# Performance work log

Hardware: AMD Instinct MI355X
Metric: run time of the kernel (lower is better)

## Reference

```python
import jax, jax.numpy as jnp
import numpy as np

B, F, D, H = 16384, 39, 16, 2   # batch, fields, embed_dim, heads
VOCAB = 10000                    # per-field vocab
DH = D * H                       # attention output dim per layer (no head split)


def setup_inputs() -> dict:
    key = jax.random.key(0)
    ks = jax.random.split(key, 32)
    def n(k, shape, s=0.05):
        return jax.random.normal(k, shape, jnp.float32) * s
    inp = {"x": jax.random.randint(ks[0], (B, F), 0, VOCAB, dtype=jnp.int32)}
    inp["emb"] = n(ks[1], (F * VOCAB, D))
    idx = 2
    for i, din in enumerate([D, DH, DH]):  # layer0: 16->32, layers 1-2: 32->32
        for nm in ["wq", "wk", "wv", "wr"]:
            inp[f"{nm}{i}"] = n(ks[idx], (din, DH)); idx += 1
    prev = F * DH  # 1248 after flatten
    for i, u in enumerate([128, 64, 32, 1], 1):
        inp[f"w{i}"] = n(ks[idx], (prev, u)); idx += 1
        inp[f"b{i}"] = jnp.zeros((u,), jnp.float32)
        prev = u
    return inp


def reference(x, emb,
              wq0, wk0, wv0, wr0,
              wq1, wk1, wv1, wr1,
              wq2, wk2, wv2, wr2,
              w1, b1, w2, b2, w3, b3, w4, b4):
    offsets = jnp.arange(F, dtype=jnp.int32) * VOCAB
    e = emb[x + offsets]                                   # [B, F, D]
    for wq, wk, wv, wr in [(wq0, wk0, wv0, wr0),
                           (wq1, wk1, wv1, wr1),
                           (wq2, wk2, wv2, wr2)]:
        q = jnp.einsum('bfd,de->bfe', e, wq)               # [B, F, DH]
        k = jnp.einsum('bfd,de->bfe', e, wk)
        v = jnp.einsum('bfd,de->bfe', e, wv)
        att = jax.nn.softmax(jnp.einsum('bfe,bge->bfg', q, k), axis=-1)  # [B,F,F], no scaling
        out = jnp.einsum('bfg,bge->bfe', att, v) + jnp.einsum('bfd,de->bfe', e, wr)
        e = jax.nn.relu(out)
    h = e.reshape(B, F * DH)
    for w, b in [(w1, b1), (w2, b2), (w3, b3)]:
        h = jax.nn.relu(h @ w + b)
    return jax.nn.sigmoid(h @ w4 + b4)                     # [B, 1]
```

## Files before the change

### kernel.cpp

```cpp
#include <hip/hip_runtime.h>
#include <math.h>

#define NF   39
#define NB   16384
#define NVOC 10000

typedef unsigned short u16;
typedef unsigned int   u32;
typedef float f32x4 __attribute__((ext_vector_type(4)));
typedef short s16x8 __attribute__((ext_vector_type(8)));

#define E3_U16   20447232u
#define NSWZ     182272

__device__ __forceinline__ u32 bfadj(float x){
    u32 u = __float_as_uint(x);
    return u + 0x7fffu + ((u >> 16) & 1u);
}
__device__ __forceinline__ u32 pk2(float a, float b){
#if __has_builtin(__builtin_amdgcn_cvt_pk_bf16_f32)
    auto t = __builtin_amdgcn_cvt_pk_bf16_f32(a, b);
    u32 r; __builtin_memcpy(&r, &t, 4); return r;
#else
    return __builtin_amdgcn_perm(bfadj(a), bfadj(b), 0x03020706u);
#endif
}
__device__ __forceinline__ u16 f2bf(float f){ return (u16)(bfadj(f) >> 16); }

__device__ __forceinline__ void wave_sync(){
    asm volatile("s_waitcnt lgkmcnt(0)" ::: "memory");
}
__device__ __forceinline__ f32x4 mfma16(s16x8 a, s16x8 b, f32x4 c){
    return __builtin_amdgcn_mfma_f32_16x16x32_bf16(a, b, c, 0, 0, 0);
}
__device__ __forceinline__ void store4(u16* p, f32x4 v){
    *(uint2*)p = make_uint2(pk2(v[0], v[1]), pk2(v[2], v[3]));
}

__global__ void __launch_bounds__(256) swz_kernel(
    const float* __restrict__ wq0, const float* __restrict__ wk0,
    const float* __restrict__ wv0, const float* __restrict__ wr0,
    const float* __restrict__ wq1, const float* __restrict__ wk1,
    const float* __restrict__ wv1, const float* __restrict__ wr1,
    const float* __restrict__ wq2, const float* __restrict__ wk2,
    const float* __restrict__ wv2, const float* __restrict__ wr2,
    const float* __restrict__ w1, const float* __restrict__ w2,
    const float* __restrict__ w3, u16* __restrict__ ws)
{
    int gid = (int)blockIdx.x*256 + (int)threadIdx.x;
    if (gid >= NSWZ) return;
    int w    = gid & 511;
    int lane = w >> 3, j = w & 7;
    int n    = lane & 15, quad = lane >> 4;
    int kin  = quad*8 + j;
    float val;
    if (gid < 12288){
        int mat = gid >> 10;
        int nt  = (gid >> 9) & 1;
        const float* W;
        switch (mat){
            case 0: W = wq0; break; case 1: W = wk0; break;
            case 2: W = wv0; break; case 3: W = wr0; break;
            case 4: W = wq1; break; case 5: W = wk1; break;
            case 6: W = wv1; break; case 7: W = wr1; break;
            case 8: W = wq2; break; case 9: W = wk2; break;
            case 10: W = wv2; break; default: W = wr2; break;
        }
        int din = (mat < 4) ? 16 : 32;
        val = (kin < din) ? W[kin*32 + nt*16 + n] : 0.f;
    } else if (gid < 12288 + 159744){
        int tt = (gid - 12288) >> 9;
        int ks = tt >> 3, nt = tt & 7;
        val = w1[(ks*32 + kin)*128 + nt*16 + n];
    } else if (gid < 12288 + 159744 + 8192){
        int tt = (gid - (12288+159744)) >> 9;
        int ks = tt >> 2, nt = tt & 3;
        val = w2[(ks*32 + kin)*64 + nt*16 + n];
    } else {
        int tt = (gid - (12288+159744+8192)) >> 9;
        int ks = tt >> 1, nt = tt & 1;
        val = w3[(ks*32 + kin)*32 + nt*16 + n];
    }
    ws[E3_U16 + gid] = f2bf(val);
}

__global__ void __launch_bounds__(256, 3) attn_kernel(
    const int* __restrict__ x, const float* __restrict__ emb,
    u16* __restrict__ ws)
{
    __shared__ __align__(16) u16 lds[4*6656];
    const int tid  = (int)threadIdx.x;
    const int wid  = tid >> 6, lane = tid & 63;
    const int h    = lane >> 4, nl = lane & 15;
    const int r    = (int)blockIdx.x*4 + wid;

    u16* eBuf = lds + wid*6656;
    u16* kBuf = eBuf + 1536;
    u16* qBuf = kBuf + 1536;
    u16* vBuf = qBuf + 1536;
    u16* pBuf = kBuf;
    const u16* wmat = ws + E3_U16;
    const f32x4 z = {0.f, 0.f, 0.f, 0.f};
    const int A_off = nl*8 + (h>>1)*128 + (h&1)*4;

    f32x4 ci;
#pragma unroll
    for (int reg = 0; reg < 4; ++reg)
        ci[reg] = (h*4 + reg >= 7) ? -1e30f : 0.f;

    if (lane < 48){
        int f = lane, mt = f >> 4, fl = f & 15;
        u16* row = eBuf + mt*512 + fl*8;
        if (f < NF){
            const float4* ep = (const float4*)(emb + ((size_t)(x[r*NF + f] + f*NVOC))*16);
            float4 e0 = ep[0], e1 = ep[1], e2 = ep[2], e3 = ep[3];
            *(uint4*)(row)       = make_uint4(pk2(e0.x,e0.y), pk2(e0.z,e0.w),
                                              pk2(e1.x,e1.y), pk2(e1.z,e1.w));
            *(uint4*)(row + 128) = make_uint4(pk2(e2.x,e2.y), pk2(e2.z,e2.w),
                                              pk2(e3.x,e3.y), pk2(e3.z,e3.w));
        } else {
            *(uint4*)(row)       = make_uint4(0,0,0,0);
            *(uint4*)(row + 128) = make_uint4(0,0,0,0);
        }
        *(uint4*)(row + 256) = make_uint4(0,0,0,0);
        *(uint4*)(row + 384) = make_uint4(0,0,0,0);
    }
    wave_sync();

#pragma unroll 1
    for (int L = 0; L < 3; ++L){
        const u16* wB = wmat + L*4096;
        s16x8 bE[3];
#pragma unroll
        for (int nt = 0; nt < 3; ++nt)
            bE[nt] = *(const s16x8*)(eBuf + nt*512 + lane*8);

        {
            s16x8 a0 = *(const s16x8*)(wB + lane*8);
            s16x8 a1 = *(const s16x8*)(wB + 512 + lane*8);
#pragma unroll
            for (int nt = 0; nt < 3; ++nt){
                store4(qBuf + nt*512       + A_off, mfma16(a0, bE[nt], z));
                store4(qBuf + nt*512 + 256 + A_off, mfma16(a1, bE[nt], z));
            }
        }
        {
            s16x8 a0 = *(const s16x8*)(wB + 1024 + lane*8);
            s16x8 a1 = *(const s16x8*)(wB + 1536 + lane*8);
#pragma unroll
            for (int nt = 0; nt < 3; ++nt){
                store4(kBuf + nt*512       + A_off, mfma16(a0, bE[nt], z));
                store4(kBuf + nt*512 + 256 + A_off, mfma16(a1, bE[nt], z));
            }
        }
        {
            s16x8 b0 = *(const s16x8*)(wB + 2048 + lane*8);
            s16x8 b1 = *(const s16x8*)(wB + 2560 + lane*8);
#pragma unroll
            for (int mtg = 0; mtg < 3; ++mtg){
                int toff = (mtg>>1)*1024 + (mtg&1)*256;
                store4(vBuf + toff       + A_off, mfma16(bE[mtg], b0, z));
                store4(vBuf + toff + 512 + A_off, mfma16(bE[mtg], b1, z));
            }
            *(uint2*)(vBuf + 2*512 + 256 + lane*4) = make_uint2(0,0);
            *(uint2*)(vBuf + 3*512 + 256 + lane*4) = make_uint2(0,0);
        }
        f32x4 R[2][3];
        {
            s16x8 a0 = *(const s16x8*)(wB + 3072 + lane*8);
            s16x8 a1 = *(const s16x8*)(wB + 3584 + lane*8);
#pragma unroll
            for (int nt = 0; nt < 3; ++nt){
                R[0][nt] = mfma16(a0, bE[nt], z);
                R[1][nt] = mfma16(a1, bE[nt], z);
            }
        }
        wave_sync();

        f32x4 S[3][3];
        {
            s16x8 aK[3], bQ[3];
#pragma unroll
            for (int i = 0; i < 3; ++i){
                aK[i] = *(const s16x8*)(kBuf + i*512 + lane*8);
                bQ[i] = *(const s16x8*)(qBuf + i*512 + lane*8);
            }
#pragma unroll
            for (int mtg = 0; mtg < 3; ++mtg)
#pragma unroll
            for (int nt = 0; nt < 3; ++nt)
                S[mtg][nt] = mfma16(aK[mtg], bQ[nt], (mtg == 2) ? ci : z);
        }
        float inv[3];
#pragma unroll
        for (int nt = 0; nt < 3; ++nt){
            float t = 0.f;
#pragma unroll
            for (int mtg = 0; mtg < 3; ++mtg)
#pragma unroll
            for (int reg = 0; reg < 4; ++reg){
                S[mtg][nt][reg] = __expf(S[mtg][nt][reg]);
                t += S[mtg][nt][reg];
            }
            t += __shfl_xor(t, 16, 64);
            t += __shfl_xor(t, 32, 64);
            inv[nt] = 1.0f / t;
        }
#pragma unroll
        for (int mtg = 0; mtg < 3; ++mtg)
#pragma unroll
        for (int nt = 0; nt < 3; ++nt)
            store4(pBuf + ((mtg>>1)*3 + nt)*512 + (mtg&1)*256 + A_off, S[mtg][nt]);
        wave_sync();

        s16x8 aV[2][2], bP[2][3];
#pragma unroll
        for (int ks = 0; ks < 2; ++ks){
#pragma unroll
            for (int emt = 0; emt < 2; ++emt)
                aV[ks][emt] = *(const s16x8*)(vBuf + (ks*2+emt)*512 + lane*8);
#pragma unroll
            for (int nt = 0; nt < 3; ++nt)
                bP[ks][nt] = *(const s16x8*)(pBuf + (ks*3+nt)*512 + lane*8);
        }
        if (L < 2){
#pragma unroll
            for (int emt = 0; emt < 2; ++emt)
#pragma unroll
            for (int nt = 0; nt < 3; ++nt){
                f32x4 o = mfma16(aV[1][emt], bP[1][nt],
                         mfma16(aV[0][emt], bP[0][nt], z));
                float m = (nt < 2 || nl < 7) ? 1.f : 0.f;
#pragma unroll
                for (int reg = 0; reg < 4; ++reg)
                    o[reg] = fmaxf(fmaf(o[reg], inv[nt], R[emt][nt][reg]), 0.f) * m;
                store4(eBuf + nt*512 + emt*256 + A_off, o);
            }
        } else {
            int st = r >> 4, sm = r & 15;
            u32 base = (u32)(st*39)*512u + (u32)(sm*8 + (h>>1)*128 + (h&1)*4);
#pragma unroll
            for (int emt = 0; emt < 2; ++emt)
#pragma unroll
            for (int nt = 0; nt < 3; ++nt){
                f32x4 o = mfma16(aV[1][emt], bP[1][nt],
                         mfma16(aV[0][emt], bP[0][nt], z));
#pragma unroll
                for (int reg = 0; reg < 4; ++reg)
                    o[reg] = fmaxf(fmaf(o[reg], inv[nt], R[emt][nt][reg]), 0.f);
                int f = nt*16 + nl;
                if (f < NF)
                    *(uint2*)(ws + base + (u32)f*512u + emt*256) =
                        make_uint2(pk2(o[0], o[1]), pk2(o[2], o[3]));
            }
        }
        wave_sync();
    }
}

__global__ void __launch_bounds__(256, 4) mlp_kernel(
    const float* __restrict__ b1, const float* __restrict__ b2,
    const float* __restrict__ b3, const float* __restrict__ w4,
    const float* __restrict__ b4, const u16* __restrict__ ws,
    float* __restrict__ out)
{
    __shared__ __align__(16) float red[8192];
    __shared__ __align__(16) u16 h1t[2048];
    __shared__ __align__(16) u16 h2t[1024];
    __shared__ float part[32];
    const int tid = (int)threadIdx.x;
    const int w   = tid >> 6, lane = tid & 63;
    const int h   = lane >> 4, nl = lane & 15;
    const int st  = (int)blockIdx.x;
    const int A_off = nl*8 + (h>>1)*128 + (h&1)*4;

    const u16* w1b = ws + E3_U16 + 12288u;
    const u16* w2b = w1b + 159744u;
    const u16* w3b = w2b + 8192u;
    const f32x4 z = {0.f,0.f,0.f,0.f};

    f32x4 acc[8];
#pragma unroll
    for (int nt = 0; nt < 8; ++nt) acc[nt] = z;
#pragma unroll 1
    for (int ks = w; ks < 39; ks += 4){
        s16x8 aE = *(const s16x8*)(ws + (u32)(st*39 + ks)*512u + lane*8);
#pragma unroll
        for (int nt = 0; nt < 8; ++nt){
            s16x8 aW = *(const s16x8*)(w1b + (ks*8 + nt)*512 + lane*8);
            acc[nt] = mfma16(aW, aE, acc[nt]);
        }
    }
#pragma unroll
    for (int nt = 0; nt < 8; ++nt)
        *(f32x4*)(red + (w*8 + nt)*256 + lane*4) = acc[nt];
    __syncthreads();

#pragma unroll
    for (int t = 0; t < 2; ++t){
        int ft = 2*w + t;
        f32x4 s = *(const f32x4*)(red + (0*8 + ft)*256 + lane*4);
#pragma unroll
        for (int p = 1; p < 4; ++p){
            f32x4 q = *(const f32x4*)(red + (p*8 + ft)*256 + lane*4);
#pragma unroll
            for (int reg = 0; reg < 4; ++reg) s[reg] += q[reg];
        }
        float4 bv = *(const float4*)(b1 + ft*16 + h*4);
        f32x4 v;
        v[0] = fmaxf(s[0] + bv.x, 0.f);
        v[1] = fmaxf(s[1] + bv.y, 0.f);
        v[2] = fmaxf(s[2] + bv.z, 0.f);
        v[3] = fmaxf(s[3] + bv.w, 0.f);
        store4(h1t + ft*256 + A_off, v);
    }
    __syncthreads();

    {
        f32x4 a2 = z;
#pragma unroll
        for (int ks = 0; ks < 4; ++ks){
            s16x8 aW = *(const s16x8*)(w2b + (ks*4 + w)*512 + lane*8);
            s16x8 bH = *(const s16x8*)(h1t + ks*512 + lane*8);
            a2 = mfma16(aW, bH, a2);
        }
        float4 bv = *(const float4*)(b2 + w*16 + h*4);
        f32x4 v;
        v[0] = fmaxf(a2[0] + bv.x, 0.f);
        v[1] = fmaxf(a2[1] + bv.y, 0.f);
        v[2] = fmaxf(a2[2] + bv.z, 0.f);
        v[3] = fmaxf(a2[3] + bv.w, 0.f);
        store4(h2t + (w>>1)*512 + (w&1)*256 + A_off, v);
    }
    __syncthreads();

    if (w < 2){
        f32x4 a3 = z;
#pragma unroll
        for (int ks = 0; ks < 2; ++ks){
            s16x8 aW = *(const s16x8*)(w3b + (ks*2 + w)*512 + lane*8);
            s16x8 bH = *(const s16x8*)(h2t + ks*512 + lane*8);
            a3 = mfma16(aW, bH, a3);
        }
        float4 b3v = *(const float4*)(b3 + w*16 + h*4);
        float4 w4v = *(const float4*)(w4 + w*16 + h*4);
        float t = fmaxf(a3[0] + b3v.x, 0.f)*w4v.x
                + fmaxf(a3[1] + b3v.y, 0.f)*w4v.y
                + fmaxf(a3[2] + b3v.z, 0.f)*w4v.z
                + fmaxf(a3[3] + b3v.w, 0.f)*w4v.w;
        t += __shfl_xor(t, 16, 64);
        t += __shfl_xor(t, 32, 64);
        if (h == 0) part[w*16 + nl] = t;
    }
    __syncthreads();
    if (tid < 16){
        float zz = part[tid] + part[16 + tid] + b4[0];
        out[st*16 + tid] = 1.f/(1.f + __expf(-zz));
    }
}

extern "C" void kernel_launch(void* const* d_in, const int* in_sizes, int n_in,
                              void* d_out, int out_size, void* d_ws, size_t ws_size,
                              hipStream_t stream)
{
    (void)in_sizes; (void)n_in; (void)ws_size; (void)out_size;
    const int*   x   = (const int*)d_in[0];
    const float* emb = (const float*)d_in[1];
    u16* ws = (u16*)d_ws;

    swz_kernel<<<(NSWZ+255)/256, 256, 0, stream>>>(
        (const float*)d_in[2],  (const float*)d_in[3],  (const float*)d_in[4],  (const float*)d_in[5],
        (const float*)d_in[6],  (const float*)d_in[7],  (const float*)d_in[8],  (const float*)d_in[9],
        (const float*)d_in[10], (const float*)d_in[11], (const float*)d_in[12], (const float*)d_in[13],
        (const float*)d_in[14], (const float*)d_in[16], (const float*)d_in[18], ws);

    attn_kernel<<<NB/4, 256, 0, stream>>>(x, emb, ws);

    mlp_kernel<<<NB/16, 256, 0, stream>>>(
        (const float*)d_in[15], (const float*)d_in[17], (const float*)d_in[19],
        (const float*)d_in[20], (const float*)d_in[21], ws, (float*)d_out);
}
```

Baseline: 192.1 us.

## Shrink attention LDS footprint, fold log2e into Wq, accumulate residual in MFMA

Overlaps the embedding buffer with the V buffer, cutting per-wave LDS from 6656 to 5120 elements so launch bounds can rise to 4 blocks per CU. Extra waits are added so the aliased buffer is not overwritten before it is read. Log2(e) is folded into the Wq weights during swizzling so softmax can use the hardware exp2, and the reciprocal uses a fast rcp. Probabilities are normalised before the PV MFMA so the residual R can seed the accumulator directly. This costs some bf16 precision on the normalised probabilities and the folded Wq.

```diff
diff --git a/kernel.cpp b/kernel.cpp
--- a/kernel.cpp
+++ b/kernel.cpp
@@ -26,6 +26,21 @@
 #endif
 }
 __device__ __forceinline__ u16 f2bf(float f){ return (u16)(bfadj(f) >> 16); }
+
+__device__ __forceinline__ float fexp2(float x){
+#if __has_builtin(__builtin_amdgcn_exp2f)
+    return __builtin_amdgcn_exp2f(x);
+#else
+    return exp2f(x);
+#endif
+}
+__device__ __forceinline__ float frcp(float x){
+#if __has_builtin(__builtin_amdgcn_rcpf)
+    return __builtin_amdgcn_rcpf(x);
+#else
+    return 1.f / x;
+#endif
+}
 
 __device__ __forceinline__ void wave_sync(){
     asm volatile("s_waitcnt lgkmcnt(0)" ::: "memory");
@@ -68,6 +83,7 @@
         }
         int din = (mat < 4) ? 16 : 32;
         val = (kin < din) ? W[kin*32 + nt*16 + n] : 0.f;
+        if ((mat & 3) == 0) val *= 1.44269504f;
     } else if (gid < 12288 + 159744){
         int tt = (gid - 12288) >> 9;
         int ks = tt >> 3, nt = tt & 7;
@@ -84,20 +100,20 @@
     ws[E3_U16 + gid] = f2bf(val);
 }
 
-__global__ void __launch_bounds__(256, 3) attn_kernel(
+__global__ void __launch_bounds__(256, 4) attn_kernel(
     const int* __restrict__ x, const float* __restrict__ emb,
     u16* __restrict__ ws)
 {
-    __shared__ __align__(16) u16 lds[4*6656];
+    __shared__ __align__(16) u16 lds[4*5120];
     const int tid  = (int)threadIdx.x;
     const int wid  = tid >> 6, lane = tid & 63;
     const int h    = lane >> 4, nl = lane & 15;
     const int r    = (int)blockIdx.x*4 + wid;
 
-    u16* eBuf = lds + wid*6656;
-    u16* kBuf = eBuf + 1536;
+    u16* vBuf = lds + wid*5120;
+    u16* eBuf = vBuf;
+    u16* kBuf = vBuf + 2048;
     u16* qBuf = kBuf + 1536;
-    u16* vBuf = qBuf + 1536;
     u16* pBuf = kBuf;
     const u16* wmat = ws + E3_U16;
     const f32x4 z = {0.f, 0.f, 0.f, 0.f};
@@ -134,6 +150,7 @@
 #pragma unroll
         for (int nt = 0; nt < 3; ++nt)
             bE[nt] = *(const s16x8*)(eBuf + nt*512 + lane*8);
+        wave_sync();
 
         {
             s16x8 a0 = *(const s16x8*)(wB + lane*8);
@@ -199,18 +216,22 @@
             for (int mtg = 0; mtg < 3; ++mtg)
 #pragma unroll
             for (int reg = 0; reg < 4; ++reg){
-                S[mtg][nt][reg] = __expf(S[mtg][nt][reg]);
+                S[mtg][nt][reg] = fexp2(S[mtg][nt][reg]);
                 t += S[mtg][nt][reg];
             }
             t += __shfl_xor(t, 16, 64);
             t += __shfl_xor(t, 32, 64);
-            inv[nt] = 1.0f / t;
+            inv[nt] = frcp(t);
         }
 #pragma unroll
         for (int mtg = 0; mtg < 3; ++mtg)
 #pragma unroll
-        for (int nt = 0; nt < 3; ++nt)
-            store4(pBuf + ((mtg>>1)*3 + nt)*512 + (mtg&1)*256 + A_off, S[mtg][nt]);
+        for (int nt = 0; nt < 3; ++nt){
+            f32x4 p;
+#pragma unroll
+            for (int reg = 0; reg < 4; ++reg) p[reg] = S[mtg][nt][reg]*inv[nt];
+            store4(pBuf + ((mtg>>1)*3 + nt)*512 + (mtg&1)*256 + A_off, p);
+        }
         wave_sync();
 
         s16x8 aV[2][2], bP[2][3];
@@ -223,17 +244,18 @@
             for (int nt = 0; nt < 3; ++nt)
                 bP[ks][nt] = *(const s16x8*)(pBuf + (ks*3+nt)*512 + lane*8);
         }
+        wave_sync();
         if (L < 2){
 #pragma unroll
             for (int emt = 0; emt < 2; ++emt)
 #pragma unroll
             for (int nt = 0; nt < 3; ++nt){
                 f32x4 o = mfma16(aV[1][emt], bP[1][nt],
-                         mfma16(aV[0][emt], bP[0][nt], z));
+                         mfma16(aV[0][emt], bP[0][nt], R[emt][nt]));
                 float m = (nt < 2 || nl < 7) ? 1.f : 0.f;
 #pragma unroll
                 for (int reg = 0; reg < 4; ++reg)
-                    o[reg] = fmaxf(fmaf(o[reg], inv[nt], R[emt][nt][reg]), 0.f) * m;
+                    o[reg] = fmaxf(o[reg], 0.f) * m;
                 store4(eBuf + nt*512 + emt*256 + A_off, o);
             }
         } else {
@@ -244,10 +266,10 @@
 #pragma unroll
             for (int nt = 0; nt < 3; ++nt){
                 f32x4 o = mfma16(aV[1][emt], bP[1][nt],
-                         mfma16(aV[0][emt], bP[0][nt], z));
+                         mfma16(aV[0][emt], bP[0][nt], R[emt][nt]));
 #pragma unroll
                 for (int reg = 0; reg < 4; ++reg)
-                    o[reg] = fmaxf(fmaf(o[reg], inv[nt], R[emt][nt][reg]), 0.f);
+                    o[reg] = fmaxf(o[reg], 0.f);
                 int f = nt*16 + nl;
                 if (f < NF)
                     *(uint2*)(ws + base + (u32)f*512u + emt*256) =
```

Result: no change. 189.6 us (-1.3%).
